# Kernel tuning notes

Measured on AMD Instinct MI355X. Metric: run time of the kernel, lower is better.

Reference implementation:

```python
import jax, jax.numpy as jnp
import numpy as np

DIM = 16
HID = 32

def setup_inputs() -> dict:
    key = jax.random.key(0)
    ks = jax.random.split(key, 5)
    B, S = 32768, 64
    x = jax.random.normal(ks[0], (B, S, DIM), dtype=jnp.float32)
    # LayerNorm params (torch defaults: weight=1, bias=0)
    ln_w = jnp.ones((DIM,), dtype=jnp.float32)
    ln_b = jnp.zeros((DIM,), dtype=jnp.float32)
    # Linear params, torch-style init scale ~ 1/sqrt(fan_in)
    w1 = jax.random.uniform(ks[1], (HID, DIM), jnp.float32, -1.0, 1.0) / np.sqrt(DIM)
    b1 = jax.random.uniform(ks[2], (HID,), jnp.float32, -1.0, 1.0) / np.sqrt(DIM)
    w2 = jax.random.uniform(ks[3], (DIM, HID), jnp.float32, -1.0, 1.0) / np.sqrt(HID)
    b2 = jax.random.uniform(ks[4], (DIM,), jnp.float32, -1.0, 1.0) / np.sqrt(HID)
    return {"x": x, "ln_w": ln_w, "ln_b": ln_b, "w1": w1, "b1": b1, "w2": w2, "b2": b2}

def _layernorm(x, w, b, eps=1e-5):
    mu = jnp.mean(x, axis=-1, keepdims=True)
    var = jnp.mean(jnp.square(x - mu), axis=-1, keepdims=True)
    return (x - mu) * jax.lax.rsqrt(var + eps) * w + b

def reference(x, ln_w, ln_b, w1, b1, w2, b2):
    h = _layernorm(x, ln_w, ln_b)
    h = jnp.einsum('bsd,hd->bsh', h, w1) + b1
    h = jax.nn.gelu(h, approximate=False)  # torch nn.GELU default is exact erf
    h = jnp.einsum('bsh,dh->bsd', h, w2) + b2
    return x + h
```

## Files before the change

kernel.cpp:

```cpp
#include <hip/hip_runtime.h>
#include <math.h>

#define DIM 16
#define HID 32

typedef float  f32x4  __attribute__((ext_vector_type(4)));
typedef short  bf16x8 __attribute__((ext_vector_type(8)));
typedef float  v2f    __attribute__((ext_vector_type(2)));

#define ROW_STRIDE_B 80
#define LDS_PER_WAVE (64 * ROW_STRIDE_B)

__device__ inline unsigned short f2bf(float f) {
    union { float f; unsigned u; } v; v.f = f;
    unsigned r = v.u + 0x7fffu + ((v.u >> 16) & 1u);
    return (unsigned short)(r >> 16);
}

__device__ inline unsigned cvt_pk_bf16(float lo, float hi) {
    unsigned r;
    asm("v_cvt_pk_bf16_f32 %0, %1, %2" : "=v"(r) : "v"(lo), "v"(hi));
    return r;
}

__device__ inline v2f gelu2(v2f h) {
    v2f hh  = h * (v2f){0.5f, 0.5f};
    v2f ahh = __builtin_elementwise_abs(hh);
    v2f az  = ahh * (v2f){1.41421356237309505f, 1.41421356237309505f};
    v2f den = __builtin_elementwise_fma(az, (v2f){0.3275911f, 0.3275911f},
                                        (v2f){1.0f, 1.0f});
    v2f t   = (v2f){__builtin_amdgcn_rcpf(den.x), __builtin_amdgcn_rcpf(den.y)};
    v2f h2  = h * h;
    v2f ex  = h2 * (v2f){-0.721347520444482f, -0.721347520444482f};
    v2f e   = (v2f){__builtin_amdgcn_exp2f(ex.x), __builtin_amdgcn_exp2f(ex.y)};
    v2f p   = __builtin_elementwise_fma(t, (v2f){1.061405429f, 1.061405429f},
                                        (v2f){-1.453152027f, -1.453152027f});
    p = __builtin_elementwise_fma(t, p, (v2f){1.421413741f, 1.421413741f});
    p = __builtin_elementwise_fma(t, p, (v2f){-0.284496736f, -0.284496736f});
    p = __builtin_elementwise_fma(t, p, (v2f){0.254829592f, 0.254829592f});
    p = p * t;
    v2f erfa = __builtin_elementwise_fma(-p, e, (v2f){1.0f, 1.0f});
    return __builtin_elementwise_fma(ahh, erfa, hh);
}

__global__ __launch_bounds__(256) void fused_ln_mlp_mfma(
    const float* __restrict__ x,
    const float* __restrict__ ln_w,
    const float* __restrict__ ln_b,
    const float* __restrict__ w1,
    const float* __restrict__ b1,
    const float* __restrict__ w2,
    const float* __restrict__ b2,
    float* __restrict__ out,
    int nrows)
{
    __shared__ __align__(16) unsigned char lds_all[4 * LDS_PER_WAVE];

    const int tid  = threadIdx.x;
    const int lane = tid & 63;
    const int wave = tid >> 6;
    const int q    = lane >> 4;
    const int c    = lane & 15;

    unsigned char* nbuf = lds_all + wave * LDS_PER_WAVE;
    const int rowbase = (blockIdx.x * 4 + wave) * 64;
    (void)nrows;

    bf16x8 aW1[2];
    #pragma unroll
    for (int t = 0; t < 2; t++) {
        bf16x8 f = {0, 0, 0, 0, 0, 0, 0, 0};
        if (q < 2) {
            const float* wp = w1 + (c + 16 * t) * DIM + q * 8;
            #pragma unroll
            for (int j = 0; j < 8; j++)
                ((unsigned short*)&f)[j] = f2bf(wp[j]);
        }
        aW1[t] = f;
    }
    bf16x8 aW2;
    {
        const float* wp = w2 + c * HID + q * 8;
        #pragma unroll
        for (int j = 0; j < 8; j++)
            ((unsigned short*)&aW2)[j] = f2bf(wp[j]);
    }
    const f32x4 b1v0 = *(const f32x4*)(b1 + 4 * q);
    const f32x4 b1v1 = *(const f32x4*)(b1 + 16 + 4 * q);
    const f32x4 b2v4 = *(const f32x4*)(b2 + 4 * q);

    const float* xr = x + (size_t)(rowbase + lane) * DIM;
    v2f xv2[8];
    {
        f32x4 t0 = *(const f32x4*)(xr + 0);
        f32x4 t1 = *(const f32x4*)(xr + 4);
        f32x4 t2 = *(const f32x4*)(xr + 8);
        f32x4 t3 = *(const f32x4*)(xr + 12);
        xv2[0] = (v2f){t0.x, t0.y}; xv2[1] = (v2f){t0.z, t0.w};
        xv2[2] = (v2f){t1.x, t1.y}; xv2[3] = (v2f){t1.z, t1.w};
        xv2[4] = (v2f){t2.x, t2.y}; xv2[5] = (v2f){t2.z, t2.w};
        xv2[6] = (v2f){t3.x, t3.y}; xv2[7] = (v2f){t3.z, t3.w};
    }
    v2f s = xv2[0] + xv2[1];
    s += xv2[2] + xv2[3];
    s += xv2[4] + xv2[5];
    s += xv2[6] + xv2[7];
    float mu = (s.x + s.y) * (1.0f / DIM);
    v2f mu2 = (v2f){mu, mu};
    v2f vs = (v2f){0.0f, 0.0f};
    #pragma unroll
    for (int i = 0; i < 8; i++) {
        v2f d = xv2[i] - mu2;
        vs = __builtin_elementwise_fma(d, d, vs);
    }
    float var = (vs.x + vs.y) * (1.0f / DIM);
    float a = __builtin_amdgcn_rsqf(var + 1e-5f);
    float cc = -mu * a;

    const v2f* lnw2 = (const v2f*)ln_w;
    const v2f* lnb2 = (const v2f*)ln_b;
    v2f a2 = (v2f){a, a};
    v2f c2 = (v2f){cc, cc};
    unsigned dw[8];
    #pragma unroll
    for (int i = 0; i < 8; i++) {
        v2f xh = __builtin_elementwise_fma(xv2[i], a2, c2);
        v2f r  = __builtin_elementwise_fma(xh, lnw2[i], lnb2[i]);
        dw[i] = cvt_pk_bf16(r.x, r.y);
    }

    {
        int4 w0, w1v, zz;
        w0.x  = (int)dw[0]; w0.y  = (int)dw[1]; w0.z  = (int)dw[2]; w0.w  = (int)dw[3];
        w1v.x = (int)dw[4]; w1v.y = (int)dw[5]; w1v.z = (int)dw[6]; w1v.w = (int)dw[7];
        zz.x = zz.y = zz.z = zz.w = 0;
        int4* rowp = (int4*)(nbuf + lane * ROW_STRIDE_B);
        rowp[0] = w0; rowp[1] = w1v; rowp[2] = zz; rowp[3] = zz;
    }
    asm volatile("s_waitcnt lgkmcnt(0)" ::: "memory");

    #pragma unroll
    for (int rc = 0; rc < 4; rc++) {
        const bf16x8 xfrag =
            *(const bf16x8*)(nbuf + (rc * 16 + c) * ROW_STRIDE_B + q * 16);
        f32x4 z = {0.f, 0.f, 0.f, 0.f};
        f32x4 h0 = __builtin_amdgcn_mfma_f32_16x16x32_bf16(aW1[0], xfrag, z, 0, 0, 0);
        f32x4 h1 = __builtin_amdgcn_mfma_f32_16x16x32_bf16(aW1[1], xfrag, z, 0, 0, 0);
        h0 += b1v0;
        h1 += b1v1;
        v2f g0 = gelu2((v2f){h0.x, h0.y});
        v2f g1 = gelu2((v2f){h0.z, h0.w});
        v2f g2 = gelu2((v2f){h1.x, h1.y});
        v2f g3 = gelu2((v2f){h1.z, h1.w});
        unsigned d0 = cvt_pk_bf16(g0.x, g0.y);
        unsigned d1 = cvt_pk_bf16(g1.x, g1.y);
        unsigned d2 = cvt_pk_bf16(g2.x, g2.y);
        unsigned d3 = cvt_pk_bf16(g3.x, g3.y);
        unsigned char* prow = nbuf + (rc * 16 + c) * ROW_STRIDE_B;
        int2 lo; lo.x = (int)d0; lo.y = (int)d1;
        int2 hi; hi.x = (int)d2; hi.y = (int)d3;
        *(int2*)(prow + 8 * q)      = lo;
        *(int2*)(prow + 32 + 8 * q) = hi;
    }
    asm volatile("s_waitcnt lgkmcnt(0)" ::: "memory");

    #pragma unroll
    for (int rc = 0; rc < 4; rc++) {
        const bf16x8 pfrag =
            *(const bf16x8*)(nbuf + (rc * 16 + c) * ROW_STRIDE_B + q * 16);
        f32x4 z = {0.f, 0.f, 0.f, 0.f};
        f32x4 y = __builtin_amdgcn_mfma_f32_16x16x32_bf16(aW2, pfrag, z, 0, 0, 0);
        size_t base = (size_t)(rowbase + rc * 16 + c) * DIM + 4 * q;
        f32x4 xres = *(const f32x4*)(x + base);
        f32x4 o = y + b2v4 + xres;
        __builtin_nontemporal_store(o, (f32x4*)(out + base));
    }
}

extern "C" void kernel_launch(void* const* d_in, const int* in_sizes, int n_in,
                              void* d_out, int out_size, void* d_ws, size_t ws_size,
                              hipStream_t stream) {
    const float* x    = (const float*)d_in[0];
    const float* ln_w = (const float*)d_in[1];
    const float* ln_b = (const float*)d_in[2];
    const float* w1   = (const float*)d_in[3];
    const float* b1   = (const float*)d_in[4];
    const float* w2   = (const float*)d_in[5];
    const float* b2   = (const float*)d_in[6];
    float* out = (float*)d_out;

    int nrows = in_sizes[0] / DIM;
    int rows_per_block = 256;
    int grid = (nrows + rows_per_block - 1) / rows_per_block;

    fused_ln_mlp_mfma<<<grid, 256, 0, stream>>>(
        x, ln_w, ln_b, w1, b1, w2, b2, out, nrows);
}
```

Before: 242.2 us.

## Eliminate LDS staging by matching MFMA fragment layouts in registers

Removes the per-wave LDS buffer. Each lane now loads x directly in the MFMA B-fragment layout and computes the LayerNorm statistics with cross-lane shuffles. The W1 and W2 fragments are permuted so the GELU output of the first MFMA feeds the second MFMA straight from registers, with no LDS write/read round-trip. The residual reuses the x already held in registers, so x is not read again from global memory. In exchange it adds shuffle reductions and computes variance as E[x²]−mu², which is slightly less numerically robust.

```diff
diff --git a/kernel.cpp b/kernel.cpp
--- a/kernel.cpp
+++ b/kernel.cpp
@@ -5,11 +5,8 @@
 #define HID 32
 
 typedef float  f32x4  __attribute__((ext_vector_type(4)));
+typedef float  v2f    __attribute__((ext_vector_type(2)));
 typedef short  bf16x8 __attribute__((ext_vector_type(8)));
-typedef float  v2f    __attribute__((ext_vector_type(2)));
-
-#define ROW_STRIDE_B 80
-#define LDS_PER_WAVE (64 * ROW_STRIDE_B)
 
 __device__ inline unsigned short f2bf(float f) {
     union { float f; unsigned u; } v; v.f = f;
@@ -54,15 +51,11 @@
     float* __restrict__ out,
     int nrows)
 {
-    __shared__ __align__(16) unsigned char lds_all[4 * LDS_PER_WAVE];
-
     const int tid  = threadIdx.x;
     const int lane = tid & 63;
     const int wave = tid >> 6;
     const int q    = lane >> 4;
     const int c    = lane & 15;
-
-    unsigned char* nbuf = lds_all + wave * LDS_PER_WAVE;
     const int rowbase = (blockIdx.x * 4 + wave) * 64;
     (void)nrows;
 
@@ -70,109 +63,73 @@
     #pragma unroll
     for (int t = 0; t < 2; t++) {
         bf16x8 f = {0, 0, 0, 0, 0, 0, 0, 0};
-        if (q < 2) {
-            const float* wp = w1 + (c + 16 * t) * DIM + q * 8;
-            #pragma unroll
-            for (int j = 0; j < 8; j++)
-                ((unsigned short*)&f)[j] = f2bf(wp[j]);
-        }
+        const float* wp = w1 + (16 * t + c) * DIM + 4 * q;
+        #pragma unroll
+        for (int j = 0; j < 4; j++)
+            ((unsigned short*)&f)[j] = f2bf(wp[j]);
         aW1[t] = f;
     }
     bf16x8 aW2;
     {
-        const float* wp = w2 + c * HID + q * 8;
+        const float* wp = w2 + c * HID;
         #pragma unroll
-        for (int j = 0; j < 8; j++)
-            ((unsigned short*)&aW2)[j] = f2bf(wp[j]);
+        for (int j = 0; j < 8; j++) {
+            int hid = (j < 4) ? (4 * q + j) : (16 + 4 * q + (j - 4));
+            ((unsigned short*)&aW2)[j] = f2bf(wp[hid]);
+        }
     }
-    const f32x4 b1v0 = *(const f32x4*)(b1 + 4 * q);
-    const f32x4 b1v1 = *(const f32x4*)(b1 + 16 + 4 * q);
-    const f32x4 b2v4 = *(const f32x4*)(b2 + 4 * q);
+    const f32x4 b1q0 = *(const f32x4*)(b1 + 4 * q);
+    const f32x4 b1q1 = *(const f32x4*)(b1 + 16 + 4 * q);
+    const f32x4 b2q  = *(const f32x4*)(b2 + 4 * q);
+    const f32x4 lnw4 = *(const f32x4*)(ln_w + 4 * q);
+    const f32x4 lnb4 = *(const f32x4*)(ln_b + 4 * q);
 
-    const float* xr = x + (size_t)(rowbase + lane) * DIM;
-    v2f xv2[8];
-    {
-        f32x4 t0 = *(const f32x4*)(xr + 0);
-        f32x4 t1 = *(const f32x4*)(xr + 4);
-        f32x4 t2 = *(const f32x4*)(xr + 8);
-        f32x4 t3 = *(const f32x4*)(xr + 12);
-        xv2[0] = (v2f){t0.x, t0.y}; xv2[1] = (v2f){t0.z, t0.w};
-        xv2[2] = (v2f){t1.x, t1.y}; xv2[3] = (v2f){t1.z, t1.w};
-        xv2[4] = (v2f){t2.x, t2.y}; xv2[5] = (v2f){t2.z, t2.w};
-        xv2[6] = (v2f){t3.x, t3.y}; xv2[7] = (v2f){t3.z, t3.w};
-    }
-    v2f s = xv2[0] + xv2[1];
-    s += xv2[2] + xv2[3];
-    s += xv2[4] + xv2[5];
-    s += xv2[6] + xv2[7];
-    float mu = (s.x + s.y) * (1.0f / DIM);
-    v2f mu2 = (v2f){mu, mu};
-    v2f vs = (v2f){0.0f, 0.0f};
+    f32x4 xv[4];
     #pragma unroll
-    for (int i = 0; i < 8; i++) {
-        v2f d = xv2[i] - mu2;
-        vs = __builtin_elementwise_fma(d, d, vs);
-    }
-    float var = (vs.x + vs.y) * (1.0f / DIM);
-    float a = __builtin_amdgcn_rsqf(var + 1e-5f);
-    float cc = -mu * a;
-
-    const v2f* lnw2 = (const v2f*)ln_w;
-    const v2f* lnb2 = (const v2f*)ln_b;
-    v2f a2 = (v2f){a, a};
-    v2f c2 = (v2f){cc, cc};
-    unsigned dw[8];
-    #pragma unroll
-    for (int i = 0; i < 8; i++) {
-        v2f xh = __builtin_elementwise_fma(xv2[i], a2, c2);
-        v2f r  = __builtin_elementwise_fma(xh, lnw2[i], lnb2[i]);
-        dw[i] = cvt_pk_bf16(r.x, r.y);
-    }
-
-    {
-        int4 w0, w1v, zz;
-        w0.x  = (int)dw[0]; w0.y  = (int)dw[1]; w0.z  = (int)dw[2]; w0.w  = (int)dw[3];
-        w1v.x = (int)dw[4]; w1v.y = (int)dw[5]; w1v.z = (int)dw[6]; w1v.w = (int)dw[7];
-        zz.x = zz.y = zz.z = zz.w = 0;
-        int4* rowp = (int4*)(nbuf + lane * ROW_STRIDE_B);
-        rowp[0] = w0; rowp[1] = w1v; rowp[2] = zz; rowp[3] = zz;
-    }
-    asm volatile("s_waitcnt lgkmcnt(0)" ::: "memory");
+    for (int rc = 0; rc < 4; rc++)
+        xv[rc] = *(const f32x4*)(x + (size_t)(rowbase + rc * 16 + c) * DIM + 4 * q);
 
     #pragma unroll
     for (int rc = 0; rc < 4; rc++) {
-        const bf16x8 xfrag =
-            *(const bf16x8*)(nbuf + (rc * 16 + c) * ROW_STRIDE_B + q * 16);
-        f32x4 z = {0.f, 0.f, 0.f, 0.f};
-        f32x4 h0 = __builtin_amdgcn_mfma_f32_16x16x32_bf16(aW1[0], xfrag, z, 0, 0, 0);
-        f32x4 h1 = __builtin_amdgcn_mfma_f32_16x16x32_bf16(aW1[1], xfrag, z, 0, 0, 0);
-        h0 += b1v0;
-        h1 += b1v1;
+        const f32x4 v = xv[rc];
+
+        float s  = (v.x + v.y) + (v.z + v.w);
+        float ss = fmaf(v.x, v.x, fmaf(v.y, v.y, fmaf(v.z, v.z, v.w * v.w)));
+        s  += __shfl_xor(s, 16);  ss += __shfl_xor(ss, 16);
+        s  += __shfl_xor(s, 32);  ss += __shfl_xor(ss, 32);
+        float mu  = s * (1.0f / DIM);
+        float var = fmaf(-mu, mu, ss * (1.0f / DIM));
+        float a   = __builtin_amdgcn_rsqf(var + 1e-5f);
+
+        f32x4 aw  = lnw4 * a;
+        f32x4 muv = {mu, mu, mu, mu};
+        f32x4 off = __builtin_elementwise_fma(-muv, aw, lnb4);
+        f32x4 xn  = __builtin_elementwise_fma(v, aw, off);
+
+        union { unsigned u[4]; bf16x8 f; } bX;
+        bX.u[0] = cvt_pk_bf16(xn.x, xn.y);
+        bX.u[1] = cvt_pk_bf16(xn.z, xn.w);
+        bX.u[2] = 0u;
+        bX.u[3] = 0u;
+
+        const f32x4 z = {0.f, 0.f, 0.f, 0.f};
+        f32x4 h0 = __builtin_amdgcn_mfma_f32_16x16x32_bf16(aW1[0], bX.f, z, 0, 0, 0) + b1q0;
+        f32x4 h1 = __builtin_amdgcn_mfma_f32_16x16x32_bf16(aW1[1], bX.f, z, 0, 0, 0) + b1q1;
+
         v2f g0 = gelu2((v2f){h0.x, h0.y});
         v2f g1 = gelu2((v2f){h0.z, h0.w});
         v2f g2 = gelu2((v2f){h1.x, h1.y});
         v2f g3 = gelu2((v2f){h1.z, h1.w});
-        unsigned d0 = cvt_pk_bf16(g0.x, g0.y);
-        unsigned d1 = cvt_pk_bf16(g1.x, g1.y);
-        unsigned d2 = cvt_pk_bf16(g2.x, g2.y);
-        unsigned d3 = cvt_pk_bf16(g3.x, g3.y);
-        unsigned char* prow = nbuf + (rc * 16 + c) * ROW_STRIDE_B;
-        int2 lo; lo.x = (int)d0; lo.y = (int)d1;
-        int2 hi; hi.x = (int)d2; hi.y = (int)d3;
-        *(int2*)(prow + 8 * q)      = lo;
-        *(int2*)(prow + 32 + 8 * q) = hi;
-    }
-    asm volatile("s_waitcnt lgkmcnt(0)" ::: "memory");
+        union { unsigned u[4]; bf16x8 f; } bP;
+        bP.u[0] = cvt_pk_bf16(g0.x, g0.y);
+        bP.u[1] = cvt_pk_bf16(g1.x, g1.y);
+        bP.u[2] = cvt_pk_bf16(g2.x, g2.y);
+        bP.u[3] = cvt_pk_bf16(g3.x, g3.y);
 
-    #pragma unroll
-    for (int rc = 0; rc < 4; rc++) {
-        const bf16x8 pfrag =
-            *(const bf16x8*)(nbuf + (rc * 16 + c) * ROW_STRIDE_B + q * 16);
-        f32x4 z = {0.f, 0.f, 0.f, 0.f};
-        f32x4 y = __builtin_amdgcn_mfma_f32_16x16x32_bf16(aW2, pfrag, z, 0, 0, 0);
+        f32x4 acc = __builtin_amdgcn_mfma_f32_16x16x32_bf16(aW2, bP.f, z, 0, 0, 0);
+
+        f32x4 o = acc + b2q + v;
         size_t base = (size_t)(rowbase + rc * 16 + c) * DIM + 4 * q;
-        f32x4 xres = *(const f32x4*)(x + base);
-        f32x4 o = y + b2v4 + xres;
         __builtin_nontemporal_store(o, (f32x4*)(out + base));
     }
 }
```

Measured after the change: 234.7 us. -3.1%, faster.
